# Performance work log

Hardware: AMD Instinct MI355X
Metric: run time of the kernel (lower is better)

The kernel has to match this reference:

```python
import jax, jax.numpy as jnp
import numpy as np
import math

N = 131072   # number of points
C = 32       # embed_dim
K = 19       # num_class
ZD = 16      # z_dim
BN_EPS = 1e-4
SIG_THR = 0.8


def setup_inputs():
    key = jax.random.key(0)
    ks = jax.random.split(key, 16)
    f32 = jnp.float32
    rn = lambda k, s, sc=1.0: jax.random.normal(k, s, dtype=f32) * sc
    return {
        'feat': rn(ks[0], (N, C)),
        'scene_flow': rn(ks[1], (N, 3)),
        'coarse_pred': rn(ks[2], (N, K)),
        'z': rn(ks[3], (ZD,)),
        'select_w1': rn(ks[4], (C, C), 0.2),
        'bn_gamma': jnp.ones((C,), f32),
        'bn_beta': jnp.zeros((C,), f32),
        'bn_mean': jnp.zeros((C,), f32),
        'bn_var': jnp.ones((C,), f32),
        'select_w2': rn(ks[5], (C, 1), 0.2),
        'select_b2': jnp.zeros((1,), f32),
        'wq': rn(ks[6], (C, C), 0.2), 'bq': jnp.zeros((C,), f32),
        'wk': rn(ks[7], (C, C), 0.2), 'bk': jnp.zeros((C,), f32),
        'wv': rn(ks[8], (C, C), 0.2), 'bv': jnp.zeros((C,), f32),
        'wo': rn(ks[9], (C, C), 0.2), 'bo': jnp.zeros((C,), f32),
        'wt': rn(ks[10], (2 * C, C), 0.2), 'bt': jnp.zeros((C,), f32),
        'w_out': rn(ks[11], (C, K), 0.2), 'b_out': jnp.zeros((K,), f32),
        'w_gen': rn(ks[12], (ZD + K + 3, C), 0.2), 'b_gen': jnp.zeros((C,), f32),
    }


def _forward(feat, scene_flow, coarse_pred, z, select_w1, bn_gamma, bn_beta,
             bn_mean, bn_var, select_w2, select_b2, wq, bq, wk, bk, wv, bv,
             wo, bo, wt, bt, w_out, b_out, w_gen, b_gen):
    cp = jax.nn.softmax(coarse_pred, axis=-1)                      # (N, K)
    temp_mask = jnp.any(scene_flow != 0, axis=-1)                  # (N,)
    # select_mlp: Linear(no bias) -> BatchNorm(eval, eps=1e-4) -> ReLU -> Linear -> Sigmoid
    h = (feat @ select_w1 - bn_mean) / jnp.sqrt(bn_var + BN_EPS) * bn_gamma + bn_beta
    h = jnp.maximum(h, 0.0)
    score = jax.nn.sigmoid(h @ select_w2 + select_b2)[:, 0]        # (N,)
    valid = (score < SIG_THR) & temp_mask                          # (N,)
    # cvae stand-in: linear over concat(z, onehot(class), scene_flow) -> (N, K, C)
    wz, wc, ws = w_gen[:ZD], w_gen[ZD:ZD + K], w_gen[ZD + K:]
    gen = (z @ wz + b_gen)[None, None, :] + wc[None, :, :] + (scene_flow @ ws)[:, None, :]
    gen = gen * cp[:, :, None]                                     # scale by softmax prob
    # tiny cross-attention: 1 query per point over K=19 class prototypes
    q = feat @ wq + bq                                             # (N, C)
    k_ = jnp.einsum('nkc,cd->nkd', gen, wk) + bk                   # (N, K, C)
    v_ = jnp.einsum('nkc,cd->nkd', gen, wv) + bv                   # (N, K, C)
    attn = jax.nn.softmax(jnp.einsum('nd,nkd->nk', q, k_) / math.sqrt(C), axis=-1)
    aug = jnp.einsum('nk,nkd->nd', attn, v_) @ wo + bo             # (N, C)
    # scatter-back: invalid points get zeros (equivalent to torch boolean scatter)
    new_feat = jnp.where(valid[:, None], aug, 0.0)
    refine = jnp.concatenate([feat, new_feat], axis=-1) @ wt + bt  # (N, C)
    return refine @ w_out + b_out                                  # (N, K)


def reference(feat, scene_flow, coarse_pred, z, select_w1, bn_gamma, bn_beta,
              bn_mean, bn_var, select_w2, select_b2, wq, bq, wk, bk, wv, bv,
              wo, bo, wt, bt, w_out, b_out, w_gen, b_gen):
    return _forward(feat, scene_flow, coarse_pred, z, select_w1, bn_gamma,
                    bn_beta, bn_mean, bn_var, select_w2, select_b2, wq, bq,
                    wk, bk, wv, bv, wo, bo, wt, bt, w_out, b_out, w_gen, b_gen)
```

## Files before the change

### kernel.cpp

```cpp
#include <hip/hip_runtime.h>

#define NPTS 131072
#define PRE_BLOCKS 16

typedef __attribute__((ext_vector_type(8))) short short8;
typedef __attribute__((ext_vector_type(4))) float f32x4;

constexpr int OFF_SW1 = 0;
constexpr int OFF_BNS = 1024;
constexpr int OFF_BNH = 1056;
constexpr int OFF_SW2 = 1088;
constexpr int OFF_B2  = 1120;
constexpr int OFF_QGB = 1121;
constexpr int OFF_QMB = 1140;
constexpr int OFF_BB  = 1143;
constexpr int OFF_CV  = 1162;
constexpr int OFF_MVB = 1181;
constexpr int EGVB    = 1240;
constexpr int FRAGH   = 1620;
constexpr int FRAGL   = 2900;

#define CONST_AS __attribute__((address_space(4)))
__device__ __forceinline__ const CONST_AS float* to_const(const float* p) {
    return (const CONST_AS float*)p;
}
__device__ __forceinline__ unsigned b16r(float x) {
    unsigned u = __float_as_uint(x);
    return (u + 0x7fffu + ((u >> 16) & 1u)) >> 16;
}
__device__ __forceinline__ float fromb(unsigned h) {
    return __uint_as_float(h << 16);
}
__device__ __forceinline__ int fragidx(int e, int col) {
    int T = col >> 4, l = (col & 15) + ((e >> 3) << 4), jj = e & 7;
    return (T * 64 + l) * 8 + jj;
}

__global__ __launch_bounds__(256) void pre_par(
    const float* __restrict__ z,
    const float* __restrict__ sw1,
    const float* __restrict__ bn_gamma, const float* __restrict__ bn_beta,
    const float* __restrict__ bn_mean,  const float* __restrict__ bn_var,
    const float* __restrict__ sw2,      const float* __restrict__ sb2,
    const float* __restrict__ wq, const float* __restrict__ bq,
    const float* __restrict__ wk, const float* __restrict__ wv,
    const float* __restrict__ bv,
    const float* __restrict__ wo, const float* __restrict__ bo,
    const float* __restrict__ wt, const float* __restrict__ bt,
    const float* __restrict__ wout, const float* __restrict__ bout,
    const float* __restrict__ wgen, const float* __restrict__ bgen,
    float* __restrict__ W)
{
    __shared__ float XA2s[608], XGs[608], XMKs[96], XMVs[96];
    __shared__ float XGKs[608], XGVs[608], XBs[608];
    const int tid = threadIdx.x;
    unsigned short* FH = (unsigned short*)(W + FRAGH);
    unsigned short* FL = (unsigned short*)(W + FRAGL);

    for (int i = tid; i < 1312; i += 256) {
        if (i < 608) {
            int e = i / 19, j = i % 19;
            float a2 = 0.f;
            for (int d = 0; d < 32; ++d) a2 += wt[(32 + e)*32 + d] * wout[d*19 + j];
            XA2s[i] = a2;
        } else if (i < 1216) {
            int t = i - 608, k = t >> 5, e = t & 31;
            float g = bgen[e];
            for (int d = 0; d < 16; ++d) g += z[d] * wgen[d*32 + e];
            XGs[t] = g + wgen[(16 + k)*32 + e];
        } else {
            int t = i - 1216, m = t >> 5, c = t & 31;
            float a = 0.f, b = 0.f;
            for (int e = 0; e < 32; ++e) {
                float wsr = wgen[(35 + m)*32 + e];
                a += wsr * wk[e*32 + c];
                b += wsr * wv[e*32 + c];
            }
            XMKs[t] = a; XMVs[t] = b;
        }
    }
    __syncthreads();
    for (int i = tid; i < 1216; i += 256) {
        if (i < 608) {
            int k = i >> 5, c = i & 31;
            float a = 0.f, b = 0.f;
            for (int e = 0; e < 32; ++e) {
                float g = XGs[k*32 + e];
                a += g * wk[e*32 + c];
                b += g * wv[e*32 + c];
            }
            XGKs[i] = a; XGVs[i] = b;
        } else {
            int t2 = i - 608, c = t2 / 19, j = t2 % 19;
            float a = 0.f;
            for (int d = 0; d < 32; ++d) a += wo[c*32 + d] * XA2s[d*19 + j];
            XBs[t2] = a;
        }
    }
    __syncthreads();
    for (int i = blockIdx.x * 256 + tid; i < 5138; i += 256 * PRE_BLOCKS) {
        if (i < 1024) {
            W[OFF_SW1 + i] = sw1[(i & 31) * 32 + (i >> 5)];
        } else if (i < 1632) {
            int t = i - 1024, e = t / 19, j = t % 19;
            float a1 = 0.f;
            for (int d = 0; d < 32; ++d) a1 += wt[e*32 + d] * wout[d*19 + j];
            FH[fragidx(e, 51 + j)] = (unsigned short)b16r(a1);
        } else if (i < 1664) {
            int t = i - 1632;
            float scale = bn_gamma[t] / sqrtf(bn_var[t] + 1e-4f);
            W[OFF_BNS + t] = scale;
            W[OFF_BNH + t] = bn_beta[t] - bn_mean[t] * scale;
            W[OFF_SW2 + t] = sw2[t];
        } else if (i < 1683) {
            int t = i - 1664;
            float a = bout[t];
            for (int d = 0; d < 32; ++d) a += bt[d] * wout[d*19 + t];
            W[OFF_BB + t] = a;
        } else if (i == 1683) {
            W[OFF_B2] = sb2[0];
        } else if (i < 2708) {
            int idx = i - 1684;
            int T = idx >> 9, rem = idx & 511, l = rem >> 3, j = rem & 7;
            int e = ((l >> 4) << 3) + j, col = 16*T + (l & 15);
            FH[(T*64 + l)*8 + j] = (unsigned short)b16r(sw1[e*32 + col]);
        } else if (i < 3732) {
            int idx = i - 2708;
            int T = idx >> 9, rem = idx & 511, l = rem >> 3, j = rem & 7;
            int e = ((l >> 4) << 3) + j, col = 16*T + (l & 15);
            float v = sw1[e*32 + col];
            FL[(T*64 + l)*8 + j] = (unsigned short)b16r(v - fromb(b16r(v)));
        } else if (i < 3956) {
            int idx = i - 3732;
            int col = 73 + idx / 32, rem = idx & 31, qq = rem >> 3, j2 = rem & 7;
            int l = (col & 15) + (qq << 4);
            FH[(4*64 + l)*8 + j2] = 0;
        } else if (i < 4052) {
            int t2 = i - 3956, e = t2 / 3, m = t2 % 3;
            float a = 0.f;
            for (int c = 0; c < 32; ++c) a += wq[e*32 + c] * XMKs[m*32 + c];
            FH[fragidx(e, 70 + m)] = (unsigned short)b16r(a);
        } else if (i < 4055) {
            int m = i - 4052;
            float a = 0.f;
            for (int c = 0; c < 32; ++c) a += bq[c] * XMKs[m*32 + c];
            W[OFF_QMB + m] = a;
        } else if (i < 4663) {
            int t2 = i - 4055, e = t2 / 19, k = t2 % 19;
            float a = 0.f;
            for (int c = 0; c < 32; ++c) a += wq[e*32 + c] * XGKs[k*32 + c];
            FH[fragidx(e, 32 + k)] = (unsigned short)b16r(a);
        } else if (i < 4682) {
            int k = i - 4663;
            float a = 0.f;
            for (int c = 0; c < 32; ++c) a += bq[c] * XGKs[k*32 + c];
            W[OFF_QGB + k] = a;
        } else if (i < 5043) {
            int t2 = i - 4682, k = t2 / 19, j = t2 % 19;
            float a = 0.f;
            for (int c = 0; c < 32; ++c) a += XGVs[k*32 + c] * XBs[c*19 + j];
            W[EGVB + k*20 + j] = a;
        } else if (i < 5062) {
            int k = i - 5043;
            W[EGVB + k*20 + 19] = 0.f;
        } else if (i < 5119) {
            int t2 = i - 5062, m = t2 / 19, j = t2 % 19;
            float a = 0.f;
            for (int c = 0; c < 32; ++c) a += XMVs[m*32 + c] * XBs[c*19 + j];
            W[OFF_MVB + t2] = a;
        } else {
            int j = i - 5119;
            float a = 0.f;
            for (int c = 0; c < 32; ++c) a += bv[c] * XBs[c*19 + j];
            for (int d = 0; d < 32; ++d) a += bo[d] * XA2s[d*19 + j];
            W[OFF_CV + j] = a;
        }
    }
}

__global__ __launch_bounds__(256, 3) void main_k(
    const float* __restrict__ feat,
    const float* __restrict__ sflow,
    const float* __restrict__ cpred,
    const float* __restrict__ Wg,
    float* __restrict__ out)
{
    const CONST_AS float* W = to_const(Wg);
    const int t = threadIdx.x, lane = t & 63, wvi = t >> 6;
    const int pblk = blockIdx.x * 256;
    const int n15 = lane & 15, q = lane >> 4;

    __shared__ __align__(16) unsigned short OH[41 * 264];
    __shared__ __align__(16) float CP[256 * 19];
    __shared__ __align__(16) float GV[380];
    __shared__ __align__(16) float SG[256];

    float4 fva[4], fvb[4];
#pragma unroll
    for (int tile = 0; tile < 4; ++tile) {
        const float* fr = feat + (long)(pblk + wvi*64 + tile*16 + n15) * 32 + q*8;
        fva[tile] = *(const float4*)fr;
        fvb[tile] = *(const float4*)(fr + 4);
    }
    const short8* FH8 = (const short8*)(Wg + FRAGH);
    const short8* FL8 = (const short8*)(Wg + FRAGL);
    short8 bh0 = FH8[0*64 + lane], bh1 = FH8[1*64 + lane];
    short8 bh2 = FH8[2*64 + lane], bh3 = FH8[3*64 + lane];
    short8 bh4 = FH8[4*64 + lane];
    short8 bl0 = FL8[0*64 + lane], bl1 = FL8[1*64 + lane];

    const long p = pblk + t;
    float s0 = sflow[p*3 + 0], s1 = sflow[p*3 + 1], s2 = sflow[p*3 + 2];

    float bns0 = W[OFF_BNS + n15],      bnh0 = W[OFF_BNH + n15],      w20 = W[OFF_SW2 + n15];
    float bns1 = W[OFF_BNS + 16 + n15], bnh1 = W[OFF_BNH + 16 + n15], w21 = W[OFF_SW2 + 16 + n15];

    if (t < 95) ((float4*)GV)[t] = ((const float4*)(Wg + EGVB))[t];

    {
        const float4* src = (const float4*)(cpred + (long)pblk * 19);
        float4* dst = (float4*)CP;
        dst[t] = src[t];
        dst[256 + t] = src[256 + t];
        dst[512 + t] = src[512 + t];
        dst[768 + t] = src[768 + t];
        if (t < 192) dst[1024 + t] = src[1024 + t];
    }
    __syncthreads();
    {
        float cp[19];
#pragma unroll
        for (int k = 0; k < 19; ++k) cp[k] = CP[t*19 + k];
        float m1 = cp[0];
#pragma unroll
        for (int k = 1; k < 19; ++k) m1 = fmaxf(m1, cp[k]);
        float sum1 = 0.f;
#pragma unroll
        for (int k = 0; k < 19; ++k) { cp[k] = __expf(cp[k] - m1); sum1 += cp[k]; }
        float r1 = 1.f / sum1;
#pragma unroll
        for (int k = 0; k < 19; ++k) CP[t*19 + k] = cp[k] * r1;
    }

#pragma unroll
    for (int tile = 0; tile < 4; ++tile) {
        const int p0 = wvi*64 + tile*16;
        float xv[8];
        xv[0]=fva[tile].x; xv[1]=fva[tile].y; xv[2]=fva[tile].z; xv[3]=fva[tile].w;
        xv[4]=fvb[tile].x; xv[5]=fvb[tile].y; xv[6]=fvb[tile].z; xv[7]=fvb[tile].w;
        short8 ah, al;
#pragma unroll
        for (int j = 0; j < 8; ++j) {
            unsigned h = b16r(xv[j]);
            ah[j] = (short)h;
            al[j] = (short)b16r(xv[j] - fromb(h));
        }
        f32x4 z4 = {0.f, 0.f, 0.f, 0.f};
        f32x4 aH0, aH1, a2_, a3_, a4_;
        aH0 = __builtin_amdgcn_mfma_f32_16x16x32_bf16(ah, bh0, z4, 0, 0, 0);
        aH0 = __builtin_amdgcn_mfma_f32_16x16x32_bf16(ah, bl0, aH0, 0, 0, 0);
        aH0 = __builtin_amdgcn_mfma_f32_16x16x32_bf16(al, bh0, aH0, 0, 0, 0);
        aH1 = __builtin_amdgcn_mfma_f32_16x16x32_bf16(ah, bh1, z4, 0, 0, 0);
        aH1 = __builtin_amdgcn_mfma_f32_16x16x32_bf16(ah, bl1, aH1, 0, 0, 0);
        aH1 = __builtin_amdgcn_mfma_f32_16x16x32_bf16(al, bh1, aH1, 0, 0, 0);
        a2_ = __builtin_amdgcn_mfma_f32_16x16x32_bf16(ah, bh2, z4, 0, 0, 0);
        a3_ = __builtin_amdgcn_mfma_f32_16x16x32_bf16(ah, bh3, z4, 0, 0, 0);
        a4_ = __builtin_amdgcn_mfma_f32_16x16x32_bf16(ah, bh4, z4, 0, 0, 0);

        float g0, g1, g2, g3;
        {
            float h0, h1;
            h0 = fmaxf(fmaf(aH0[0], bns0, bnh0), 0.f);
            h1 = fmaxf(fmaf(aH1[0], bns1, bnh1), 0.f);
            g0 = fmaf(h0, w20, h1 * w21);
            h0 = fmaxf(fmaf(aH0[1], bns0, bnh0), 0.f);
            h1 = fmaxf(fmaf(aH1[1], bns1, bnh1), 0.f);
            g1 = fmaf(h0, w20, h1 * w21);
            h0 = fmaxf(fmaf(aH0[2], bns0, bnh0), 0.f);
            h1 = fmaxf(fmaf(aH1[2], bns1, bnh1), 0.f);
            g2 = fmaf(h0, w20, h1 * w21);
            h0 = fmaxf(fmaf(aH0[3], bns0, bnh0), 0.f);
            h1 = fmaxf(fmaf(aH1[3], bns1, bnh1), 0.f);
            g3 = fmaf(h0, w20, h1 * w21);
        }
#pragma unroll
        for (int m = 1; m < 16; m <<= 1) {
            g0 += __shfl_xor(g0, m, 64);
            g1 += __shfl_xor(g1, m, 64);
            g2 += __shfl_xor(g2, m, 64);
            g3 += __shfl_xor(g3, m, 64);
        }
        if (n15 == 0)
            *(float4*)&SG[p0 + q*4] = make_float4(g0, g1, g2, g3);

        {
            unsigned d0, d1;
            d0 = b16r(a2_[0]) | (b16r(a2_[1]) << 16);
            d1 = b16r(a2_[2]) | (b16r(a2_[3]) << 16);
            *(uint2*)&OH[(n15) * 264 + p0 + q*4] = make_uint2(d0, d1);
            d0 = b16r(a3_[0]) | (b16r(a3_[1]) << 16);
            d1 = b16r(a3_[2]) | (b16r(a3_[3]) << 16);
            *(uint2*)&OH[(16 + n15) * 264 + p0 + q*4] = make_uint2(d0, d1);
            if (n15 <= 8) {
                d0 = b16r(a4_[0]) | (b16r(a4_[1]) << 16);
                d1 = b16r(a4_[2]) | (b16r(a4_[3]) << 16);
                *(uint2*)&OH[(32 + n15) * 264 + p0 + q*4] = make_uint2(d0, d1);
            }
        }
    }
    __syncthreads();

    bool tmask = (s0 != 0.f) | (s1 != 0.f) | (s2 != 0.f);

    const float TH = 1.3862943611198906f;
    float sacc = SG[t] + W[OFF_B2];
    bool nearthr = fabsf(sacc - TH) < 1e-3f;
    if (__ballot(nearthr) != 0ULL) {
        float f[32];
        const float4* fp4 = (const float4*)(feat + p*32);
#pragma unroll
        for (int g = 0; g < 8; ++g) {
            float4 v = fp4[g];
            f[g*4+0]=v.x; f[g*4+1]=v.y; f[g*4+2]=v.z; f[g*4+3]=v.w;
        }
        float sr = W[OFF_B2];
        for (int c = 0; c < 32; ++c) {
            float a = 0.f;
#pragma unroll
            for (int e = 0; e < 32; ++e) a = fmaf(f[e], W[OFF_SW1 + c*32 + e], a);
            float h = fmaxf(fmaf(a, W[OFF_BNS + c], W[OFF_BNH + c]), 0.f);
            sr = fmaf(h, W[OFF_SW2 + c], sr);
        }
        sacc = nearthr ? sr : sacc;
    }
    bool valid = tmask && (sacc < TH);

    float qm0 = fromb(OH[38*264 + t]) + W[OFF_QMB + 0];
    float qm1 = fromb(OH[39*264 + t]) + W[OFF_QMB + 1];
    float qm2 = fromb(OH[40*264 + t]) + W[OFF_QMB + 2];
    float qs = s0*qm0 + s1*qm1 + s2*qm2;

    float cp[19];
#pragma unroll
    for (int k = 0; k < 19; ++k) cp[k] = CP[t*19 + k];

    const float RS = 0.17677669529663687f;
    float l[19];
#pragma unroll
    for (int k = 0; k < 19; ++k)
        l[k] = (cp[k] * (fromb(OH[k*264 + t]) + W[OFF_QGB + k] + qs)) * RS;

    float m2 = l[0];
#pragma unroll
    for (int k = 1; k < 19; ++k) m2 = fmaxf(m2, l[k]);
    float sum2 = 0.f;
#pragma unroll
    for (int k = 0; k < 19; ++k) { l[k] = __expf(l[k] - m2); sum2 += l[k]; }
    float r2 = 1.f / sum2;
    float Sw = 0.f;
#pragma unroll
    for (int k = 0; k < 19; ++k) { l[k] = l[k] * r2 * cp[k]; Sw += l[k]; }

    float rv[19];
    float c0 = Sw * s0, c1 = Sw * s1, c2 = Sw * s2;
    float vg = valid ? 1.f : 0.f;
    float a2v[19];
#pragma unroll
    for (int j = 0; j < 19; ++j)
        a2v[j] = W[OFF_CV + j] + c0 * W[OFF_MVB + j]
               + c1 * W[OFF_MVB + 19 + j] + c2 * W[OFF_MVB + 38 + j];
#pragma unroll
    for (int k = 0; k < 19; ++k) {
        float lk = l[k];
#pragma unroll
        for (int j = 0; j < 19; ++j) a2v[j] = fmaf(lk, GV[k*20 + j], a2v[j]);
    }
#pragma unroll
    for (int j = 0; j < 19; ++j)
        rv[j] = fmaf(vg, a2v[j], fromb(OH[(19 + j)*264 + t]) + W[OFF_BB + j]);

    __syncthreads();
    float* SLAB = (float*)OH;
#pragma unroll
    for (int j = 0; j < 19; ++j) SLAB[t*19 + j] = rv[j];
    __syncthreads();
    {
        const float4* src = (const float4*)SLAB;
        float4* dst = (float4*)(out + (long)pblk * 19);
        dst[t] = src[t];
        dst[256 + t] = src[256 + t];
        dst[512 + t] = src[512 + t];
        dst[768 + t] = src[768 + t];
        if (t < 192) dst[1024 + t] = src[1024 + t];
    }
}

extern "C" void kernel_launch(void* const* d_in, const int* in_sizes, int n_in,
                              void* d_out, int out_size, void* d_ws, size_t ws_size,
                              hipStream_t stream) {
    const float* feat  = (const float*)d_in[0];
    const float* sflow = (const float*)d_in[1];
    const float* cpred = (const float*)d_in[2];
    const float* z     = (const float*)d_in[3];
    const float* sw1   = (const float*)d_in[4];
    const float* bn_g  = (const float*)d_in[5];
    const float* bn_b  = (const float*)d_in[6];
    const float* bn_m  = (const float*)d_in[7];
    const float* bn_v  = (const float*)d_in[8];
    const float* sw2   = (const float*)d_in[9];
    const float* sb2   = (const float*)d_in[10];
    const float* wq    = (const float*)d_in[11];
    const float* bq    = (const float*)d_in[12];
    const float* wk    = (const float*)d_in[13];
    const float* bk    = (const float*)d_in[14];  (void)bk;
    const float* wv    = (const float*)d_in[15];
    const float* bv    = (const float*)d_in[16];
    const float* wo    = (const float*)d_in[17];
    const float* bo    = (const float*)d_in[18];
    const float* wt    = (const float*)d_in[19];
    const float* bt    = (const float*)d_in[20];
    const float* wout  = (const float*)d_in[21];
    const float* bout  = (const float*)d_in[22];
    const float* wgen  = (const float*)d_in[23];
    const float* bgen  = (const float*)d_in[24];

    float* W = (float*)d_ws;

    hipLaunchKernelGGL(pre_par, dim3(PRE_BLOCKS), dim3(256), 0, stream,
                       z, sw1, bn_g, bn_b, bn_m, bn_v, sw2, sb2,
                       wq, bq, wk, wv, bv, wo, bo, wt, bt, wout, bout,
                       wgen, bgen, W);

    hipLaunchKernelGGL(main_k, dim3(512), dim3(256), 0, stream,
                       feat, sflow, cpred, W, (float*)d_out);
}
```

Measured before the change: 148.0 us.

## Stage select-MLP hidden activations in LDS and keep softmax probs in registers

Replaces the per-tile BN/ReLU/shuffle reduction with storing the two fp32 MFMA accumulators into a shared slab, after which each thread reduces its own point's 32 hidden values serially. The coarse-pred softmax is computed up front and held in registers instead of being written back to LDS, and that same slab is reused for the cpred staging, the hidden values and the output. The feature loads move into the tile loop, and launch bounds drop from 3 to 2 blocks per SM. The aim is to remove the cross-lane shuffles, but the larger LDS footprint and lower occupancy hint may reduce latency hiding.

```diff
diff --git a/kernel.cpp b/kernel.cpp
--- a/kernel.cpp
+++ b/kernel.cpp
@@ -178,7 +178,7 @@
     }
 }
 
-__global__ __launch_bounds__(256, 3) void main_k(
+__global__ __launch_bounds__(256, 2) void main_k(
     const float* __restrict__ feat,
     const float* __restrict__ sflow,
     const float* __restrict__ cpred,
@@ -188,20 +188,37 @@
     const CONST_AS float* W = to_const(Wg);
     const int t = threadIdx.x, lane = t & 63, wvi = t >> 6;
     const int pblk = blockIdx.x * 256;
-    const int n15 = lane & 15, q = lane >> 4;
-
+
+    __shared__ __align__(16) float R0[32 * 264];
     __shared__ __align__(16) unsigned short OH[41 * 264];
-    __shared__ __align__(16) float CP[256 * 19];
     __shared__ __align__(16) float GV[380];
-    __shared__ __align__(16) float SG[256];
-
-    float4 fva[4], fvb[4];
-#pragma unroll
-    for (int tile = 0; tile < 4; ++tile) {
-        const float* fr = feat + (long)(pblk + wvi*64 + tile*16 + n15) * 32 + q*8;
-        fva[tile] = *(const float4*)fr;
-        fvb[tile] = *(const float4*)(fr + 4);
-    }
+
+    if (t < 95) ((float4*)GV)[t] = ((const float4*)(Wg + EGVB))[t];
+
+    {
+        const float4* src = (const float4*)(cpred + (long)pblk * 19);
+        float4* dst = (float4*)R0;
+        dst[t] = src[t];
+        dst[256 + t] = src[256 + t];
+        dst[512 + t] = src[512 + t];
+        dst[768 + t] = src[768 + t];
+        if (t < 192) dst[1024 + t] = src[1024 + t];
+    }
+    __syncthreads();
+    float cp[19];
+#pragma unroll
+    for (int k = 0; k < 19; ++k) cp[k] = R0[t*19 + k];
+    float m1 = cp[0];
+#pragma unroll
+    for (int k = 1; k < 19; ++k) m1 = fmaxf(m1, cp[k]);
+    float sum1 = 0.f;
+#pragma unroll
+    for (int k = 0; k < 19; ++k) { cp[k] = __expf(cp[k] - m1); sum1 += cp[k]; }
+    float r1 = 1.f / sum1;
+#pragma unroll
+    for (int k = 0; k < 19; ++k) cp[k] *= r1;
+    __syncthreads();
+
     const short8* FH8 = (const short8*)(Wg + FRAGH);
     const short8* FL8 = (const short8*)(Wg + FRAGL);
     short8 bh0 = FH8[0*64 + lane], bh1 = FH8[1*64 + lane];
@@ -209,45 +226,19 @@
     short8 bh4 = FH8[4*64 + lane];
     short8 bl0 = FL8[0*64 + lane], bl1 = FL8[1*64 + lane];
 
-    const long p = pblk + t;
-    float s0 = sflow[p*3 + 0], s1 = sflow[p*3 + 1], s2 = sflow[p*3 + 2];
-
-    float bns0 = W[OFF_BNS + n15],      bnh0 = W[OFF_BNH + n15],      w20 = W[OFF_SW2 + n15];
-    float bns1 = W[OFF_BNS + 16 + n15], bnh1 = W[OFF_BNH + 16 + n15], w21 = W[OFF_SW2 + 16 + n15];
-
-    if (t < 95) ((float4*)GV)[t] = ((const float4*)(Wg + EGVB))[t];
-
-    {
-        const float4* src = (const float4*)(cpred + (long)pblk * 19);
-        float4* dst = (float4*)CP;
-        dst[t] = src[t];
-        dst[256 + t] = src[256 + t];
-        dst[512 + t] = src[512 + t];
-        dst[768 + t] = src[768 + t];
-        if (t < 192) dst[1024 + t] = src[1024 + t];
-    }
-    __syncthreads();
-    {
-        float cp[19];
-#pragma unroll
-        for (int k = 0; k < 19; ++k) cp[k] = CP[t*19 + k];
-        float m1 = cp[0];
-#pragma unroll
-        for (int k = 1; k < 19; ++k) m1 = fmaxf(m1, cp[k]);
-        float sum1 = 0.f;
-#pragma unroll
-        for (int k = 0; k < 19; ++k) { cp[k] = __expf(cp[k] - m1); sum1 += cp[k]; }
-        float r1 = 1.f / sum1;
-#pragma unroll
-        for (int k = 0; k < 19; ++k) CP[t*19 + k] = cp[k] * r1;
-    }
+    const int n15 = lane & 15, q = lane >> 4;
 
 #pragma unroll
     for (int tile = 0; tile < 4; ++tile) {
         const int p0 = wvi*64 + tile*16;
+        const float* fr = feat + (long)(pblk + p0 + n15) * 32 + q*8;
         float xv[8];
-        xv[0]=fva[tile].x; xv[1]=fva[tile].y; xv[2]=fva[tile].z; xv[3]=fva[tile].w;
-        xv[4]=fvb[tile].x; xv[5]=fvb[tile].y; xv[6]=fvb[tile].z; xv[7]=fvb[tile].w;
+        {
+            float4 va = *(const float4*)fr;
+            float4 vb = *(const float4*)(fr + 4);
+            xv[0]=va.x; xv[1]=va.y; xv[2]=va.z; xv[3]=va.w;
+            xv[4]=vb.x; xv[5]=vb.y; xv[6]=vb.z; xv[7]=vb.w;
+        }
         short8 ah, al;
 #pragma unroll
         for (int j = 0; j < 8; ++j) {
@@ -267,32 +258,8 @@
         a3_ = __builtin_amdgcn_mfma_f32_16x16x32_bf16(ah, bh3, z4, 0, 0, 0);
         a4_ = __builtin_amdgcn_mfma_f32_16x16x32_bf16(ah, bh4, z4, 0, 0, 0);
 
-        float g0, g1, g2, g3;
-        {
-            float h0, h1;
-            h0 = fmaxf(fmaf(aH0[0], bns0, bnh0), 0.f);
-            h1 = fmaxf(fmaf(aH1[0], bns1, bnh1), 0.f);
-            g0 = fmaf(h0, w20, h1 * w21);
-            h0 = fmaxf(fmaf(aH0[1], bns0, bnh0), 0.f);
-            h1 = fmaxf(fmaf(aH1[1], bns1, bnh1), 0.f);
-            g1 = fmaf(h0, w20, h1 * w21);
-            h0 = fmaxf(fmaf(aH0[2], bns0, bnh0), 0.f);
-            h1 = fmaxf(fmaf(aH1[2], bns1, bnh1), 0.f);
-            g2 = fmaf(h0, w20, h1 * w21);
-            h0 = fmaxf(fmaf(aH0[3], bns0, bnh0), 0.f);
-            h1 = fmaxf(fmaf(aH1[3], bns1, bnh1), 0.f);
-            g3 = fmaf(h0, w20, h1 * w21);
-        }
-#pragma unroll
-        for (int m = 1; m < 16; m <<= 1) {
-            g0 += __shfl_xor(g0, m, 64);
-            g1 += __shfl_xor(g1, m, 64);
-            g2 += __shfl_xor(g2, m, 64);
-            g3 += __shfl_xor(g3, m, 64);
-        }
-        if (n15 == 0)
-            *(float4*)&SG[p0 + q*4] = make_float4(g0, g1, g2, g3);
-
+        *(f32x4*)&R0[(n15)      * 264 + p0 + q*4] = aH0;
+        *(f32x4*)&R0[(16 + n15) * 264 + p0 + q*4] = aH1;
         {
             unsigned d0, d1;
             d0 = b16r(a2_[0]) | (b16r(a2_[1]) << 16);
@@ -310,10 +277,19 @@
     }
     __syncthreads();
 
+    const long p = pblk + t;
+
+    float s0 = sflow[p*3 + 0], s1 = sflow[p*3 + 1], s2 = sflow[p*3 + 2];
     bool tmask = (s0 != 0.f) | (s1 != 0.f) | (s2 != 0.f);
 
     const float TH = 1.3862943611198906f;
-    float sacc = SG[t] + W[OFF_B2];
+    float sacc = W[OFF_B2];
+#pragma unroll
+    for (int c = 0; c < 32; ++c) {
+        float a = R0[c*264 + t];
+        float h = fmaxf(fmaf(a, W[OFF_BNS + c], W[OFF_BNH + c]), 0.f);
+        sacc = fmaf(h, W[OFF_SW2 + c], sacc);
+    }
     bool nearthr = fabsf(sacc - TH) < 1e-3f;
     if (__ballot(nearthr) != 0ULL) {
         float f[32];
@@ -340,10 +316,6 @@
     float qm2 = fromb(OH[40*264 + t]) + W[OFF_QMB + 2];
     float qs = s0*qm0 + s1*qm1 + s2*qm2;
 
-    float cp[19];
-#pragma unroll
-    for (int k = 0; k < 19; ++k) cp[k] = CP[t*19 + k];
-
     const float RS = 0.17677669529663687f;
     float l[19];
 #pragma unroll
@@ -380,12 +352,11 @@
         rv[j] = fmaf(vg, a2v[j], fromb(OH[(19 + j)*264 + t]) + W[OFF_BB + j]);
 
     __syncthreads();
-    float* SLAB = (float*)OH;
-#pragma unroll
-    for (int j = 0; j < 19; ++j) SLAB[t*19 + j] = rv[j];
+#pragma unroll
+    for (int j = 0; j < 19; ++j) R0[t*19 + j] = rv[j];
     __syncthreads();
     {
-        const float4* src = (const float4*)SLAB;
+        const float4* src = (const float4*)R0;
         float4* dst = (float4*)(out + (long)pblk * 19);
         dst[t] = src[t];
         dst[256 + t] = src[256 + t];
```

Measured after the change: 144.0 us. 1.03x faster.
